# Optimization experiments

Measured on AMD Instinct MI355X. Metric: run time of the kernel, lower is better.

## Reference

```python
import jax, jax.numpy as jnp
import numpy as np

B, N, DEG, F_IN, D = 32, 1024, 16, 8, 64

def setup_inputs() -> dict:
    key = jax.random.key(0)
    ks = jax.random.split(key, 24)
    T = B * N
    E = B * N * DEG
    x = jax.random.normal(ks[0], (T, F_IN), dtype=jnp.float32)
    # edges confined within each graph (block-diagonal batched graph)
    off = (jnp.arange(B) * N)[:, None]
    src = jax.random.randint(ks[1], (B, N * DEG), 0, N) + off
    dst = jax.random.randint(ks[2], (B, N * DEG), 0, N) + off
    edge_index = jnp.stack([src.reshape(-1), dst.reshape(-1)]).astype(jnp.int64)
    reachable = jax.random.randint(ks[3], (T,), 0, 2, dtype=jnp.int32)
    s = 0.1
    p = lambda k, shp: jax.random.normal(k, shp, dtype=jnp.float32) * s
    return {
        'x': x, 'edge_index': edge_index, 'reachable': reachable,
        'Wl0': p(ks[4], (D, F_IN)), 'Wr0': p(ks[5], (D, F_IN)),
        'att0': p(ks[6], (D,)), 'b0': p(ks[7], (D,)),
        'Wl': p(ks[8], (4, D, D)), 'Wr': p(ks[9], (4, D, D)),
        'att': p(ks[10], (4, D)), 'b': p(ks[11], (4, D)),
        't6w': p(ks[12], (D, D)), 't6b': p(ks[13], (D,)),
        't7w': p(ks[14], (D, D)), 't7b': p(ks[15], (D,)),
        't5pw': p(ks[16], (1, 2 * D)), 't5pb': p(ks[17], (1,)),
        't5vw': p(ks[18], (1, 2 * D)), 't5vb': p(ks[19], (1,)),
        'pw': p(ks[20], (1, 1)), 'pb': p(ks[21], (1,)),
        'vw': p(ks[22], (1, 1)), 'vb': p(ks[23], (1,)),
        'n_per_graph': N,
    }

def reference(x, edge_index, reachable, Wl0, Wr0, att0, b0, Wl, Wr, att, b,
              t6w, t6b, t7w, t7b, t5pw, t5pb, t5vw, t5vb, pw, pb, vw, vb,
              n_per_graph):
    T = x.shape[0]
    n = int(n_per_graph)
    bsz = T // n
    d = Wl0.shape[0]
    # GATv2Conv adds self loops by default
    loop = jnp.arange(T)
    src = jnp.concatenate([edge_index[0], loop])
    dst = jnp.concatenate([edge_index[1], loop])

    def gatv2(h, WlK, WrK, a, bb):
        xl = h @ WlK.T                                  # [T, d]
        xr = h @ WrK.T
        e = jax.nn.leaky_relu(xl[src] + xr[dst], 0.2) @ a  # [E]
        emax = jax.ops.segment_max(e, dst, num_segments=T)
        ee = jnp.exp(e - emax[dst])
        denom = jax.ops.segment_sum(ee, dst, num_segments=T)
        alpha = ee / denom[dst]                         # edge softmax per target
        return jax.ops.segment_sum(alpha[:, None] * xl[src], dst, num_segments=T) + bb

    h = gatv2(x, Wl0, Wr0, att0, b0)
    for k in range(Wl.shape[0]):  # ReLU between layers, none after last
        h = gatv2(jax.nn.relu(h), Wl[k], Wr[k], att[k], b[k])
    mu_raw = h                                          # [T, d]

    # scatter_mean pooling per graph + repeat_interleave back to nodes
    mu_mp = mu_raw.reshape(bsz, n, d).mean(axis=1)      # [B, d]
    mu_mp_exp = jnp.repeat(mu_mp, n, axis=0)            # [T, d]

    g = mu_mp_exp @ t6w.T + t6b
    l = mu_raw @ t7w.T + t7b
    rep = jax.nn.relu(jnp.concatenate([g, l], axis=1))  # [T, 2d]

    prob_logits = rep @ t5pw.T + t5pb                   # [T, 1]
    logits = (prob_logits * pw[0, 0] + pb[0]).reshape(bsz, n, 1)

    q = (rep @ t5vw.T + t5vb)[:, 0]                     # [T]
    q = jnp.where(reachable.astype(bool), q, jnp.float32(-1e20))
    v = q.reshape(bsz, n).max(axis=1, keepdims=True)    # [B, 1]
    value = v * vw[0, 0] + vb[0]
    return logits, value
```

## Files before the change

### kernel.cpp

```cpp
#include <hip/hip_runtime.h>
#include <hip/hip_bf16.h>

typedef unsigned short u16;

#define T_NODES 32768
#define NPG 1024
#define BGR 32
#define D 64
#define FIN 8
#define SLOTS 64

typedef __attribute__((ext_vector_type(8))) short short8v;
typedef __attribute__((ext_vector_type(4))) float floatx4;
typedef __attribute__((ext_vector_type(2))) float f32x2;

__device__ __forceinline__ float bf2f(u16 u){ return __uint_as_float(((unsigned)u) << 16); }
__device__ __forceinline__ u16 f2bf(float f){
    __hip_bfloat16 h = __float2bfloat16(f);
    return *reinterpret_cast<u16*>(&h);
}
__device__ __forceinline__ f32x2 lo_hi(unsigned w){
    f32x2 r;
    r[0] = __uint_as_float(w << 16);
    r[1] = __uint_as_float(w & 0xffff0000u);
    return r;
}
__device__ __forceinline__ f32x2 lrelu2(f32x2 v){
    return __builtin_elementwise_max(v, v * 0.2f);
}
__device__ __forceinline__ short8v pack_bf8(float4 a, float4 b){
    short8v r;
    r[0]=(short)f2bf(a.x); r[1]=(short)f2bf(a.y);
    r[2]=(short)f2bf(a.z); r[3]=(short)f2bf(a.w);
    r[4]=(short)f2bf(b.x); r[5]=(short)f2bf(b.y);
    r[6]=(short)f2bf(b.z); r[7]=(short)f2bf(b.w);
    return r;
}

__device__ __forceinline__ unsigned fenc(float f){
    unsigned b = __float_as_uint(f);
    return (b & 0x80000000u) ? ~b : (b | 0x80000000u);
}
__device__ __forceinline__ float fdec(unsigned k){
    unsigned b = (k & 0x80000000u) ? (k ^ 0x80000000u) : ~k;
    return __uint_as_float(b);
}

template<int CTRL, int RM, int BM>
__device__ __forceinline__ float dpp_add(float x){
    int y = __builtin_amdgcn_update_dpp(0, __float_as_int(x), CTRL, RM, BM, false);
    return x + __int_as_float(y);
}
__device__ __forceinline__ float wave_sum63(float x){
    x = dpp_add<0x111,0xf,0xf>(x);
    x = dpp_add<0x112,0xf,0xf>(x);
    x = dpp_add<0x114,0xf,0xe>(x);
    x = dpp_add<0x118,0xf,0xc>(x);
    x = dpp_add<0x142,0xa,0xf>(x);
    x = dpp_add<0x143,0xc,0xf>(x);
    return x;
}
__device__ __forceinline__ float wave_sum_bcast(float x){
    return __int_as_float(__builtin_amdgcn_readlane(__float_as_int(wave_sum63(x)), 63));
}
__device__ __forceinline__ float row_ror_add(float x){
    x = dpp_add<0x121,0xf,0xf>(x);
    x = dpp_add<0x122,0xf,0xf>(x);
    x = dpp_add<0x124,0xf,0xf>(x);
    x = dpp_add<0x128,0xf,0xf>(x);
    return x;
}

__device__ __forceinline__ void edge_body(uint2 uv, bool valid,
        f32x2 a01, f32x2 a23, f32x2 xr01, f32x2 xr23,
        f32x2& acc01, f32x2& acc23, float& l){
    f32x2 x01 = lo_hi(uv.x);
    f32x2 x23 = lo_hi(uv.y);
    f32x2 v01 = lrelu2(x01 + xr01);
    f32x2 v23 = lrelu2(x23 + xr23);
    f32x2 e2 = v01 * a01 + v23 * a23;
    float e = e2[0] + e2[1];
    e = row_ror_add(e);
    float q = valid ? __expf(e) : 0.f;
    acc01 += q * x01;
    acc23 += q * x23;
    l += q;
}

__device__ __forceinline__ void node_edge(const u16* __restrict__ xlin,
        const int* __restrict__ colSh, int eb, int t, int deg, int sub4,
        f32x2 a01, f32x2 a23, f32x2 xr01, f32x2 xr23,
        f32x2& acc01, f32x2& acc23, float& l){
    int nEdge = deg + 1;
    for (int j0 = 0; j0 < nEdge; j0 += 8){
        uint2 u[8];
        #pragma unroll
        for (int i = 0; i < 8; i++){
            int j = j0 + i;
            int jc = (j < nEdge) ? j : (nEdge-1);
            int s = (jc < deg) ? colSh[eb + jc] : t;
            u[i] = *(const uint2*)&xlin[((size_t)(unsigned)s << 6) + sub4];
        }
        #pragma unroll
        for (int i = 0; i < 8; i++)
            edge_body(u[i], j0 + i < nEdge, a01, a23, xr01, xr23, acc01, acc23, l);
    }
}

__global__ void countscat_kernel(const int* __restrict__ src, const int* __restrict__ dst,
                                 int* __restrict__ counts, int* __restrict__ col64, int E){
    int i = blockIdx.x*blockDim.x + threadIdx.x;
    if (i < E){
        int d = dst[i];
        int slot = atomicAdd(&counts[d], 1);
        if (slot < SLOTS) col64[((size_t)d << 6) + slot] = src[i];
    }
}

__global__ void lin0_kernel(const float* __restrict__ x, const float* __restrict__ Wl0,
                            const float* __restrict__ Wr0,
                            u16* __restrict__ xlb, u16* __restrict__ xrb,
                            int* __restrict__ counts, float* __restrict__ muAcc,
                            unsigned* __restrict__ vslot, int* __restrict__ done){
    __shared__ float wl[D][FIN+1];
    __shared__ float wr[D][FIN+1];
    __shared__ float xs[32][FIN];
    int tid = threadIdx.x;
    int blk = blockIdx.x;
    int gidx = blk*256 + tid;
    if (gidx < T_NODES) counts[gidx] = 0;
    if (gidx < BGR*D)   muAcc[gidx] = 0.f;
    if (gidx < BGR){ vslot[gidx] = 0u; done[gidx] = 0; }
    int rowBase = (blk & 7)*4096 + (blk >> 3)*32;
    for (int i = tid; i < D*FIN; i += 256){
        wl[i>>3][i&7] = Wl0[i];
        wr[i>>3][i&7] = Wr0[i];
    }
    xs[tid>>3][tid&7] = x[rowBase*FIN + tid];
    __syncthreads();
    int wave = tid >> 6, lane = tid & 63;
    int rb = rowBase + wave*8;
    #pragma unroll
    for (int r = 0; r < 8; r++){
        float al = 0.f, ar = 0.f;
        int lr = wave*8 + r;
        #pragma unroll
        for (int k = 0; k < FIN; k++){
            float xv = xs[lr][k];
            al = fmaf(xv, wl[lane][k], al);
            ar = fmaf(xv, wr[lane][k], ar);
        }
        xlb[(size_t)(rb+r)*D + lane] = f2bf(al);
        xrb[(size_t)(rb+r)*D + lane] = f2bf(ar);
    }
}

__global__ __launch_bounds__(256) void el_kernel(
        const u16* __restrict__ xlin, const u16* __restrict__ xrin,
        const float* __restrict__ att, const float* __restrict__ bias,
        const int* __restrict__ counts, const int* __restrict__ col64,
        const float* __restrict__ Wl, const float* __restrict__ Wr,
        u16* __restrict__ xlout, u16* __restrict__ xrout){
    __shared__ __align__(16) u16 hs[16][80];
    __shared__ __align__(16) int colSh[16*SLOTS];
    __shared__ int cnt[16];
    int tid = threadIdx.x, blk = blockIdx.x;
    int rowBase = (blk & 7)*4096 + (blk >> 3)*16;
    if (tid < 16){
        int c = counts[rowBase + tid];
        cnt[tid] = c < SLOTS ? c : SLOTS;
    }
    *(int4*)&colSh[tid*4] = *(const int4*)&col64[((size_t)rowBase << 6) + tid*4];
    __syncthreads();
    int wave = tid >> 6, lane = tid & 63;
    int g = lane >> 4, sub4 = (lane & 15) << 2;
    int ln = wave*4 + g;
    int t  = rowBase + ln;
    f32x2 a01 = { att[sub4],   att[sub4+1] };
    f32x2 a23 = { att[sub4+2], att[sub4+3] };
    float4 b4 = *(const float4*)&bias[sub4];
    uint2 xru = *(const uint2*)&xrin[((size_t)t << 6) + sub4];
    f32x2 xr01 = lo_hi(xru.x), xr23 = lo_hi(xru.y);
    int deg = cnt[ln];
    f32x2 acc01 = {0.f,0.f}, acc23 = {0.f,0.f};
    float l = 0.f;
    node_edge(xlin, colSh, ln*SLOTS, t, deg, sub4,
              a01, a23, xr01, xr23, acc01, acc23, l);
    float rl = __frcp_rn(l);
    ushort4 hb;
    hb.x = f2bf(fmaxf(fmaf(acc01[0], rl, b4.x), 0.f));
    hb.y = f2bf(fmaxf(fmaf(acc01[1], rl, b4.y), 0.f));
    hb.z = f2bf(fmaxf(fmaf(acc23[0], rl, b4.z), 0.f));
    hb.w = f2bf(fmaxf(fmaf(acc23[1], rl, b4.w), 0.f));
    *(ushort4*)&hs[ln][sub4] = hb;
    int lw = lane & 15, lg = lane >> 4, kb = lg*8;
    int colw = (wave << 4) + lw;
    const float* wl0 = &Wl[colw*D + kb];
    const float* wr0 = &Wr[colw*D + kb];
    short8v bl0 = pack_bf8(*(const float4*)wl0,        *(const float4*)(wl0+4));
    short8v bl1 = pack_bf8(*(const float4*)(wl0+32),   *(const float4*)(wl0+36));
    short8v br0 = pack_bf8(*(const float4*)wr0,        *(const float4*)(wr0+4));
    short8v br1 = pack_bf8(*(const float4*)(wr0+32),   *(const float4*)(wr0+36));
    __syncthreads();
    short8v a0 = *(const short8v*)&hs[lw][kb];
    short8v a1 = *(const short8v*)&hs[lw][32 + kb];
    floatx4 cl = {0.f,0.f,0.f,0.f}, cr = {0.f,0.f,0.f,0.f};
    cl = __builtin_amdgcn_mfma_f32_16x16x32_bf16(a0, bl0, cl, 0, 0, 0);
    cl = __builtin_amdgcn_mfma_f32_16x16x32_bf16(a1, bl1, cl, 0, 0, 0);
    cr = __builtin_amdgcn_mfma_f32_16x16x32_bf16(a0, br0, cr, 0, 0, 0);
    cr = __builtin_amdgcn_mfma_f32_16x16x32_bf16(a1, br1, cr, 0, 0, 0);
    size_t rb = (size_t)(rowBase + lg*4);
    #pragma unroll
    for (int j = 0; j < 4; j++){
        xlout[(rb + j)*D + colw] = f2bf(cl[j]);
        xrout[(rb + j)*D + colw] = f2bf(cr[j]);
    }
}

__global__ __launch_bounds__(256) void e4_kernel(
        const u16* __restrict__ xlin, const u16* __restrict__ xrin,
        const float* __restrict__ att, const float* __restrict__ bias,
        const int* __restrict__ counts, const int* __restrict__ col64,
        float* __restrict__ hout, float* __restrict__ muAcc){
    __shared__ __align__(16) int colSh[16*SLOTS];
    __shared__ int cnt[16];
    __shared__ float red[16][D];
    int tid = threadIdx.x, blk = blockIdx.x;
    int rowBase = (blk & 7)*4096 + (blk >> 3)*16;
    if (tid < 16){
        int c = counts[rowBase + tid];
        cnt[tid] = c < SLOTS ? c : SLOTS;
    }
    *(int4*)&colSh[tid*4] = *(const int4*)&col64[((size_t)rowBase << 6) + tid*4];
    __syncthreads();
    int wave = tid >> 6, lane = tid & 63;
    int g = lane >> 4, sub4 = (lane & 15) << 2;
    int ln = wave*4 + g;
    int t  = rowBase + ln;
    f32x2 a01 = { att[sub4],   att[sub4+1] };
    f32x2 a23 = { att[sub4+2], att[sub4+3] };
    float4 b4 = *(const float4*)&bias[sub4];
    uint2 xru = *(const uint2*)&xrin[((size_t)t << 6) + sub4];
    f32x2 xr01 = lo_hi(xru.x), xr23 = lo_hi(xru.y);
    int deg = cnt[ln];
    f32x2 acc01 = {0.f,0.f}, acc23 = {0.f,0.f};
    float l = 0.f;
    node_edge(xlin, colSh, ln*SLOTS, t, deg, sub4,
              a01, a23, xr01, xr23, acc01, acc23, l);
    float rl = __frcp_rn(l);
    float4 hv;
    hv.x = fmaf(acc01[0], rl, b4.x);
    hv.y = fmaf(acc01[1], rl, b4.y);
    hv.z = fmaf(acc23[0], rl, b4.z);
    hv.w = fmaf(acc23[1], rl, b4.w);
    *(float4*)&hout[(size_t)t*D + sub4] = hv;
    *(float4*)&red[ln][sub4] = hv;
    __syncthreads();
    if (wave == 0){
        float s = 0.f;
        #pragma unroll
        for (int n = 0; n < 16; n++) s += red[n][lane];
        atomicAdd(&muAcc[(rowBase >> 10)*D + lane], s);
    }
}

__global__ __launch_bounds__(256) void final_kernel(const float* __restrict__ h,
                             const float* __restrict__ muAcc,
                             const float* __restrict__ t6w, const float* __restrict__ t6b,
                             const float* __restrict__ t7w, const float* __restrict__ t7b,
                             const float* __restrict__ t5pw, const float* __restrict__ t5pb,
                             const float* __restrict__ t5vw, const float* __restrict__ t5vb,
                             const float* __restrict__ pw, const float* __restrict__ pb,
                             const float* __restrict__ vw, const float* __restrict__ vb,
                             const int* __restrict__ reachable,
                             unsigned* __restrict__ vslot, int* __restrict__ done,
                             float* __restrict__ out_logits, float* __restrict__ out_value){
    __shared__ __align__(16) float hs[D][68];
    __shared__ __align__(16) float ws[D][68];
    __shared__ float ppar[D][17];
    __shared__ float qpar[D][17];
    __shared__ float PgQg[2];
    int tid = threadIdx.x;
    int blk = blockIdx.x;
    int rowBase = (blk & 7)*4096 + (blk >> 3)*64;
    int b = rowBase >> 10;
    for (int i = tid; i < D*D; i += 256) ws[i>>6][i&63] = t6w[i];
    if (tid < D) hs[0][tid] = muAcc[b*D + tid] * (1.f/NPG);
    __syncthreads();
    if (tid < D){
        int d = tid;
        float g = t6b[d];
        #pragma unroll
        for (int k = 0; k < D; k++) g = fmaf(hs[0][k], ws[d][k], g);
        g = fmaxf(g, 0.f);
        float pp = wave_sum_bcast(g * t5pw[d]);
        float qq = wave_sum_bcast(g * t5vw[d]);
        if (d == 0){ PgQg[0] = pp; PgQg[1] = qq; }
    }
    __syncthreads();
    for (int i = tid; i < D*D; i += 256){
        int r = i >> 6, c = i & 63;
        hs[r][c] = h[(size_t)rowBase*D + i];
        ws[r][c] = t7w[i];
    }
    __syncthreads();
    int ty = tid >> 4, tx = tid & 15;
    int r0 = ty * 4;
    float acc[4][4];
    #pragma unroll
    for (int i = 0; i < 4; i++)
        #pragma unroll
        for (int j = 0; j < 4; j++) acc[i][j] = 0.f;
    for (int k = 0; k < D; k += 4){
        float4 hv[4], wv[4];
        #pragma unroll
        for (int i = 0; i < 4; i++){
            hv[i] = *(const float4*)&hs[r0+i][k];
            wv[i] = *(const float4*)&ws[tx + 16*i][k];
        }
        #pragma unroll
        for (int i = 0; i < 4; i++)
            #pragma unroll
            for (int j = 0; j < 4; j++)
                acc[i][j] += hv[i].x*wv[j].x + hv[i].y*wv[j].y
                           + hv[i].z*wv[j].z + hv[i].w*wv[j].w;
    }
    float bc[4], pwc[4], qwc[4];
    #pragma unroll
    for (int j = 0; j < 4; j++){
        int c = tx + 16*j;
        bc[j]  = t7b[c];
        pwc[j] = t5pw[D + c];
        qwc[j] = t5vw[D + c];
    }
    #pragma unroll
    for (int i = 0; i < 4; i++){
        float sp = 0.f, sq = 0.f;
        #pragma unroll
        for (int j = 0; j < 4; j++){
            float lv = fmaxf(acc[i][j] + bc[j], 0.f);
            sp = fmaf(lv, pwc[j], sp);
            sq = fmaf(lv, qwc[j], sq);
        }
        ppar[r0+i][tx] = sp;
        qpar[r0+i][tx] = sq;
    }
    __syncthreads();
    if (tid < 64){
        int t = rowBase + tid;
        float sp = 0.f, sq = 0.f;
        #pragma unroll
        for (int c = 0; c < 16; c++){ sp += ppar[tid][c]; sq += qpar[tid][c]; }
        float prob = PgQg[0] + sp + t5pb[0];
        out_logits[t] = prob * pw[0] + pb[0];
        float q = PgQg[1] + sq + t5vb[0];
        if (!reachable[t]) q = -1e20f;
        float m = q;
        #pragma unroll
        for (int o = 1; o < 64; o <<= 1) m = fmaxf(m, __shfl_xor(m, o, 64));
        if (tid == 0){
            atomicMax(&vslot[b], fenc(m));
            __threadfence();
            int ticket = atomicAdd(&done[b], 1);
            if (ticket == (NPG/64) - 1){
                unsigned k = atomicOr(&vslot[b], 0u);
                out_value[b] = fdec(k)*vw[0] + vb[0];
            }
        }
    }
}

extern "C" void kernel_launch(void* const* d_in, const int* in_sizes, int n_in,
                              void* d_out, int out_size, void* d_ws, size_t ws_size,
                              hipStream_t stream){
    const float* x          = (const float*)d_in[0];
    const int*   edge_index = (const int*)d_in[1];
    const int*   reachable  = (const int*)d_in[2];
    const float* Wl0 = (const float*)d_in[3];
    const float* Wr0 = (const float*)d_in[4];
    const float* att0= (const float*)d_in[5];
    const float* b0  = (const float*)d_in[6];
    const float* Wl  = (const float*)d_in[7];
    const float* Wr  = (const float*)d_in[8];
    const float* att = (const float*)d_in[9];
    const float* bb  = (const float*)d_in[10];
    const float* t6w = (const float*)d_in[11];
    const float* t6b = (const float*)d_in[12];
    const float* t7w = (const float*)d_in[13];
    const float* t7b = (const float*)d_in[14];
    const float* t5pw= (const float*)d_in[15];
    const float* t5pb= (const float*)d_in[16];
    const float* t5vw= (const float*)d_in[17];
    const float* t5vb= (const float*)d_in[18];
    const float* pw  = (const float*)d_in[19];
    const float* pb  = (const float*)d_in[20];
    const float* vw  = (const float*)d_in[21];
    const float* vb  = (const float*)d_in[22];

    int E = in_sizes[1] / 2;
    const int* esrc = edge_index;
    const int* edst = edge_index + E;

    char* ws = (char*)d_ws;
    float* h    = (float*)(ws);
    u16* xlbA   = (u16*)(ws + (size_t)T_NODES*D*4);
    u16* xrbA   = (u16*)((char*)xlbA + (size_t)T_NODES*D*2);
    u16* xlbB   = (u16*)((char*)xrbA + (size_t)T_NODES*D*2);
    u16* xrbB   = (u16*)((char*)xlbB + (size_t)T_NODES*D*2);
    int* counts = (int*)((char*)xrbB + (size_t)T_NODES*D*2);
    int* col64  = (int*)((char*)counts + (size_t)(T_NODES+16)*4);
    float* muAcc= (float*)((char*)col64 + (size_t)T_NODES*SLOTS*4);
    unsigned* vslot = (unsigned*)((char*)muAcc + (size_t)BGR*D*4);
    int* done   = (int*)((char*)vslot + (size_t)BGR*4);

    lin0_kernel<<<T_NODES/32, 256, 0, stream>>>(x, Wl0, Wr0, xlbA, xrbA,
                                                counts, muAcc, vslot, done);
    countscat_kernel<<<(E+255)/256, 256, 0, stream>>>(esrc, edst, counts, col64, E);

    el_kernel<<<T_NODES/16, 256, 0, stream>>>(xlbA, xrbA, att0, b0, counts, col64,
                                              Wl + 0*D*D, Wr + 0*D*D, xlbB, xrbB);
    el_kernel<<<T_NODES/16, 256, 0, stream>>>(xlbB, xrbB, att + 0*D, bb + 0*D, counts, col64,
                                              Wl + 1*D*D, Wr + 1*D*D, xlbA, xrbA);
    el_kernel<<<T_NODES/16, 256, 0, stream>>>(xlbA, xrbA, att + 1*D, bb + 1*D, counts, col64,
                                              Wl + 2*D*D, Wr + 2*D*D, xlbB, xrbB);
    el_kernel<<<T_NODES/16, 256, 0, stream>>>(xlbB, xrbB, att + 2*D, bb + 2*D, counts, col64,
                                              Wl + 3*D*D, Wr + 3*D*D, xlbA, xrbA);
    e4_kernel<<<T_NODES/16, 256, 0, stream>>>(xlbA, xrbA, att + 3*D, bb + 3*D, counts, col64,
                                              h, muAcc);

    final_kernel<<<T_NODES/64, 256, 0, stream>>>(h, muAcc, t6w, t6b, t7w, t7b,
                                                 t5pw, t5pb, t5vw, t5vb, pw, pb, vw, vb,
                                                 reachable, vslot, done,
                                                 (float*)d_out, (float*)d_out + T_NODES);
}
```

Measured before the change: 242.9 us.

## Fuse last GAT layer with readout head using inter-block per-graph flag sync

Merges the final GATv2 layer kernel with the readout kernel so each block of 64 nodes keeps its layer output in shared memory, instead of writing h to global memory and reading it back. The per-graph mean-pool result is computed by the last-arriving block of each graph, which publishes the global projection through a flag that the other blocks spin on. This removes one launch and the h round trip. In exchange it relies on all blocks of a graph being co-resident to avoid deadlock, and it cuts block count and raises shared memory per block.

```diff
diff --git a/kernel.cpp b/kernel.cpp
--- a/kernel.cpp
+++ b/kernel.cpp
@@ -88,7 +88,7 @@
 }
 
 __device__ __forceinline__ void node_edge(const u16* __restrict__ xlin,
-        const int* __restrict__ colSh, int eb, int t, int deg, int sub4,
+        const int* colSh, int eb, int t, int deg, int sub4,
         f32x2 a01, f32x2 a23, f32x2 xr01, f32x2 xr23,
         f32x2& acc01, f32x2& acc23, float& l){
     int nEdge = deg + 1;
@@ -121,7 +121,8 @@
                             const float* __restrict__ Wr0,
                             u16* __restrict__ xlb, u16* __restrict__ xrb,
                             int* __restrict__ counts, float* __restrict__ muAcc,
-                            unsigned* __restrict__ vslot, int* __restrict__ done){
+                            unsigned* __restrict__ vslot, int* __restrict__ done,
+                            int* __restrict__ pgdone, int* __restrict__ pgflag){
     __shared__ float wl[D][FIN+1];
     __shared__ float wr[D][FIN+1];
     __shared__ float xs[32][FIN];
@@ -130,7 +131,7 @@
     int gidx = blk*256 + tid;
     if (gidx < T_NODES) counts[gidx] = 0;
     if (gidx < BGR*D)   muAcc[gidx] = 0.f;
-    if (gidx < BGR){ vslot[gidx] = 0u; done[gidx] = 0; }
+    if (gidx < BGR){ vslot[gidx] = 0u; done[gidx] = 0; pgdone[gidx] = 0; pgflag[gidx] = 0; }
     int rowBase = (blk & 7)*4096 + (blk >> 3)*32;
     for (int i = tid; i < D*FIN; i += 256){
         wl[i>>3][i&7] = Wl0[i];
@@ -217,93 +218,101 @@
     }
 }
 
-__global__ __launch_bounds__(256) void e4_kernel(
+__global__ __launch_bounds__(256) void e4final_kernel(
         const u16* __restrict__ xlin, const u16* __restrict__ xrin,
         const float* __restrict__ att, const float* __restrict__ bias,
         const int* __restrict__ counts, const int* __restrict__ col64,
-        float* __restrict__ hout, float* __restrict__ muAcc){
-    __shared__ __align__(16) int colSh[16*SLOTS];
-    __shared__ int cnt[16];
-    __shared__ float red[16][D];
+        const float* __restrict__ t6w, const float* __restrict__ t6b,
+        const float* __restrict__ t7w, const float* __restrict__ t7b,
+        const float* __restrict__ t5pw, const float* __restrict__ t5pb,
+        const float* __restrict__ t5vw, const float* __restrict__ t5vb,
+        const float* __restrict__ pw, const float* __restrict__ pb,
+        const float* __restrict__ vw, const float* __restrict__ vb,
+        const int* __restrict__ reachable,
+        float* __restrict__ muAcc, unsigned* __restrict__ vslot,
+        int* __restrict__ done, int* __restrict__ pgdone,
+        int* __restrict__ pgflag, float* __restrict__ gPQ,
+        float* __restrict__ out_logits, float* __restrict__ out_value){
+    __shared__ __align__(16) char arena[43776];
+    __shared__ float muS[D];
+    __shared__ float PgQgS[2];
+    __shared__ int isLastS;
+    float* hfin  = (float*)arena;
+    int*   colSh = (int*)  (arena + 17408);
+    int*   cnt   = (int*)  (arena + 33792);
+    float* wsH   = (float*)(arena + 17408);
+    float* ppar  = (float*)(arena + 34816);
+    float* qpar  = (float*)(arena + 39168);
+
     int tid = threadIdx.x, blk = blockIdx.x;
-    int rowBase = (blk & 7)*4096 + (blk >> 3)*16;
-    if (tid < 16){
+    int rowBase = (blk & 7)*4096 + (blk >> 3)*64;
+    int b = rowBase >> 10;
+    if (tid < 64){
         int c = counts[rowBase + tid];
         cnt[tid] = c < SLOTS ? c : SLOTS;
     }
-    *(int4*)&colSh[tid*4] = *(const int4*)&col64[((size_t)rowBase << 6) + tid*4];
+    for (int i = tid; i < 1024; i += 256)
+        *(int4*)&colSh[i*4] = *(const int4*)&col64[((size_t)rowBase << 6) + i*4];
     __syncthreads();
     int wave = tid >> 6, lane = tid & 63;
     int g = lane >> 4, sub4 = (lane & 15) << 2;
-    int ln = wave*4 + g;
-    int t  = rowBase + ln;
+    int gid = wave*4 + g;
     f32x2 a01 = { att[sub4],   att[sub4+1] };
     f32x2 a23 = { att[sub4+2], att[sub4+3] };
     float4 b4 = *(const float4*)&bias[sub4];
-    uint2 xru = *(const uint2*)&xrin[((size_t)t << 6) + sub4];
-    f32x2 xr01 = lo_hi(xru.x), xr23 = lo_hi(xru.y);
-    int deg = cnt[ln];
-    f32x2 acc01 = {0.f,0.f}, acc23 = {0.f,0.f};
-    float l = 0.f;
-    node_edge(xlin, colSh, ln*SLOTS, t, deg, sub4,
-              a01, a23, xr01, xr23, acc01, acc23, l);
-    float rl = __frcp_rn(l);
-    float4 hv;
-    hv.x = fmaf(acc01[0], rl, b4.x);
-    hv.y = fmaf(acc01[1], rl, b4.y);
-    hv.z = fmaf(acc23[0], rl, b4.z);
-    hv.w = fmaf(acc23[1], rl, b4.w);
-    *(float4*)&hout[(size_t)t*D + sub4] = hv;
-    *(float4*)&red[ln][sub4] = hv;
-    __syncthreads();
+    for (int n = 0; n < 4; n++){
+        int ln = gid + n*16;
+        int t  = rowBase + ln;
+        uint2 xru = *(const uint2*)&xrin[((size_t)t << 6) + sub4];
+        f32x2 xr01 = lo_hi(xru.x), xr23 = lo_hi(xru.y);
+        int deg = cnt[ln];
+        f32x2 acc01 = {0.f,0.f}, acc23 = {0.f,0.f};
+        float l = 0.f;
+        node_edge(xlin, colSh, ln*SLOTS, t, deg, sub4,
+                  a01, a23, xr01, xr23, acc01, acc23, l);
+        float rl = __frcp_rn(l);
+        float4 hv;
+        hv.x = fmaf(acc01[0], rl, b4.x);
+        hv.y = fmaf(acc01[1], rl, b4.y);
+        hv.z = fmaf(acc23[0], rl, b4.z);
+        hv.w = fmaf(acc23[1], rl, b4.w);
+        *(float4*)&hfin[ln*68 + sub4] = hv;
+    }
+    __syncthreads();
+    for (int i = tid; i < D*D; i += 256) wsH[(i>>6)*68 + (i&63)] = t7w[i];
     if (wave == 0){
         float s = 0.f;
         #pragma unroll
-        for (int n = 0; n < 16; n++) s += red[n][lane];
-        atomicAdd(&muAcc[(rowBase >> 10)*D + lane], s);
-    }
-}
-
-__global__ __launch_bounds__(256) void final_kernel(const float* __restrict__ h,
-                             const float* __restrict__ muAcc,
-                             const float* __restrict__ t6w, const float* __restrict__ t6b,
-                             const float* __restrict__ t7w, const float* __restrict__ t7b,
-                             const float* __restrict__ t5pw, const float* __restrict__ t5pb,
-                             const float* __restrict__ t5vw, const float* __restrict__ t5vb,
-                             const float* __restrict__ pw, const float* __restrict__ pb,
-                             const float* __restrict__ vw, const float* __restrict__ vb,
-                             const int* __restrict__ reachable,
-                             unsigned* __restrict__ vslot, int* __restrict__ done,
-                             float* __restrict__ out_logits, float* __restrict__ out_value){
-    __shared__ __align__(16) float hs[D][68];
-    __shared__ __align__(16) float ws[D][68];
-    __shared__ float ppar[D][17];
-    __shared__ float qpar[D][17];
-    __shared__ float PgQg[2];
-    int tid = threadIdx.x;
-    int blk = blockIdx.x;
-    int rowBase = (blk & 7)*4096 + (blk >> 3)*64;
-    int b = rowBase >> 10;
-    for (int i = tid; i < D*D; i += 256) ws[i>>6][i&63] = t6w[i];
-    if (tid < D) hs[0][tid] = muAcc[b*D + tid] * (1.f/NPG);
-    __syncthreads();
-    if (tid < D){
-        int d = tid;
-        float g = t6b[d];
-        #pragma unroll
-        for (int k = 0; k < D; k++) g = fmaf(hs[0][k], ws[d][k], g);
-        g = fmaxf(g, 0.f);
-        float pp = wave_sum_bcast(g * t5pw[d]);
-        float qq = wave_sum_bcast(g * t5vw[d]);
-        if (d == 0){ PgQg[0] = pp; PgQg[1] = qq; }
-    }
-    __syncthreads();
-    for (int i = tid; i < D*D; i += 256){
-        int r = i >> 6, c = i & 63;
-        hs[r][c] = h[(size_t)rowBase*D + i];
-        ws[r][c] = t7w[i];
-    }
-    __syncthreads();
+        for (int nn = 0; nn < 64; nn++) s += hfin[nn*68 + lane];
+        atomicAdd(&muAcc[b*D + lane], s);
+    }
+    __syncthreads();
+    if (tid == 0){
+        int tk = atomicAdd(&pgdone[b], 1);
+        isLastS = (tk == (NPG/64) - 1);
+    }
+    __syncthreads();
+    if (isLastS){
+        if (tid < D)
+            muS[tid] = __hip_atomic_load(&muAcc[b*D + tid], __ATOMIC_RELAXED,
+                                         __HIP_MEMORY_SCOPE_AGENT) * (1.f/NPG);
+        __syncthreads();
+        if (tid < D){
+            int d = tid;
+            float gg = t6b[d];
+            #pragma unroll
+            for (int k = 0; k < D; k++) gg = fmaf(muS[k], t6w[d*D + k], gg);
+            gg = fmaxf(gg, 0.f);
+            float pp = wave_sum_bcast(gg * t5pw[d]);
+            float qq = wave_sum_bcast(gg * t5vw[d]);
+            if (d == 0){
+                __hip_atomic_store(&gPQ[b*2],   pp, __ATOMIC_RELAXED, __HIP_MEMORY_SCOPE_AGENT);
+                __hip_atomic_store(&gPQ[b*2+1], qq, __ATOMIC_RELAXED, __HIP_MEMORY_SCOPE_AGENT);
+                asm volatile("s_waitcnt vmcnt(0)" ::: "memory");
+                __hip_atomic_store(&pgflag[b], 1, __ATOMIC_RELAXED, __HIP_MEMORY_SCOPE_AGENT);
+            }
+        }
+    }
     int ty = tid >> 4, tx = tid & 15;
     int r0 = ty * 4;
     float acc[4][4];
@@ -315,8 +324,8 @@
         float4 hv[4], wv[4];
         #pragma unroll
         for (int i = 0; i < 4; i++){
-            hv[i] = *(const float4*)&hs[r0+i][k];
-            wv[i] = *(const float4*)&ws[tx + 16*i][k];
+            hv[i] = *(const float4*)&hfin[(r0+i)*68 + k];
+            wv[i] = *(const float4*)&wsH[(tx + 16*i)*68 + k];
         }
         #pragma unroll
         for (int i = 0; i < 4; i++)
@@ -342,28 +351,37 @@
             sp = fmaf(lv, pwc[j], sp);
             sq = fmaf(lv, qwc[j], sq);
         }
-        ppar[r0+i][tx] = sp;
-        qpar[r0+i][tx] = sq;
+        ppar[(r0+i)*17 + tx] = sp;
+        qpar[(r0+i)*17 + tx] = sq;
+    }
+    __syncthreads();
+    if (tid == 0){
+        while (__hip_atomic_load(&pgflag[b], __ATOMIC_RELAXED,
+                                 __HIP_MEMORY_SCOPE_AGENT) == 0)
+            __builtin_amdgcn_s_sleep(16);
+        PgQgS[0] = __hip_atomic_load(&gPQ[b*2],   __ATOMIC_RELAXED, __HIP_MEMORY_SCOPE_AGENT);
+        PgQgS[1] = __hip_atomic_load(&gPQ[b*2+1], __ATOMIC_RELAXED, __HIP_MEMORY_SCOPE_AGENT);
     }
     __syncthreads();
     if (tid < 64){
         int t = rowBase + tid;
         float sp = 0.f, sq = 0.f;
         #pragma unroll
-        for (int c = 0; c < 16; c++){ sp += ppar[tid][c]; sq += qpar[tid][c]; }
-        float prob = PgQg[0] + sp + t5pb[0];
+        for (int c = 0; c < 16; c++){ sp += ppar[tid*17 + c]; sq += qpar[tid*17 + c]; }
+        float prob = PgQgS[0] + sp + t5pb[0];
         out_logits[t] = prob * pw[0] + pb[0];
-        float q = PgQg[1] + sq + t5vb[0];
+        float q = PgQgS[1] + sq + t5vb[0];
         if (!reachable[t]) q = -1e20f;
         float m = q;
         #pragma unroll
         for (int o = 1; o < 64; o <<= 1) m = fmaxf(m, __shfl_xor(m, o, 64));
         if (tid == 0){
             atomicMax(&vslot[b], fenc(m));
-            __threadfence();
+            asm volatile("s_waitcnt vmcnt(0)" ::: "memory");
             int ticket = atomicAdd(&done[b], 1);
             if (ticket == (NPG/64) - 1){
-                unsigned k = atomicOr(&vslot[b], 0u);
+                unsigned k = __hip_atomic_load(&vslot[b], __ATOMIC_RELAXED,
+                                               __HIP_MEMORY_SCOPE_AGENT);
                 out_value[b] = fdec(k)*vw[0] + vb[0];
             }
         }
@@ -402,19 +420,22 @@
     const int* edst = edge_index + E;
 
     char* ws = (char*)d_ws;
-    float* h    = (float*)(ws);
-    u16* xlbA   = (u16*)(ws + (size_t)T_NODES*D*4);
-    u16* xrbA   = (u16*)((char*)xlbA + (size_t)T_NODES*D*2);
-    u16* xlbB   = (u16*)((char*)xrbA + (size_t)T_NODES*D*2);
-    u16* xrbB   = (u16*)((char*)xlbB + (size_t)T_NODES*D*2);
-    int* counts = (int*)((char*)xrbB + (size_t)T_NODES*D*2);
-    int* col64  = (int*)((char*)counts + (size_t)(T_NODES+16)*4);
-    float* muAcc= (float*)((char*)col64 + (size_t)T_NODES*SLOTS*4);
-    unsigned* vslot = (unsigned*)((char*)muAcc + (size_t)BGR*D*4);
-    int* done   = (int*)((char*)vslot + (size_t)BGR*4);
+    u16* xlbA   = (u16*)ws;
+    u16* xrbA   = xlbA + (size_t)T_NODES*D;
+    u16* xlbB   = xrbA + (size_t)T_NODES*D;
+    u16* xrbB   = xlbB + (size_t)T_NODES*D;
+    int* counts = (int*)(xrbB + (size_t)T_NODES*D);
+    int* col64  = counts + T_NODES + 16;
+    float* muAcc= (float*)(col64 + (size_t)T_NODES*SLOTS);
+    unsigned* vslot = (unsigned*)(muAcc + BGR*D);
+    int* done   = (int*)(vslot + BGR);
+    int* pgdone = done + BGR;
+    int* pgflag = pgdone + BGR;
+    float* gPQ  = (float*)(pgflag + BGR);
 
     lin0_kernel<<<T_NODES/32, 256, 0, stream>>>(x, Wl0, Wr0, xlbA, xrbA,
-                                                counts, muAcc, vslot, done);
+                                                counts, muAcc, vslot, done,
+                                                pgdone, pgflag);
     countscat_kernel<<<(E+255)/256, 256, 0, stream>>>(esrc, edst, counts, col64, E);
 
     el_kernel<<<T_NODES/16, 256, 0, stream>>>(xlbA, xrbA, att0, b0, counts, col64,
@@ -425,11 +446,11 @@
                                               Wl + 2*D*D, Wr + 2*D*D, xlbB, xrbB);
     el_kernel<<<T_NODES/16, 256, 0, stream>>>(xlbB, xrbB, att + 2*D, bb + 2*D, counts, col64,
                                               Wl + 3*D*D, Wr + 3*D*D, xlbA, xrbA);
-    e4_kernel<<<T_NODES/16, 256, 0, stream>>>(xlbA, xrbA, att + 3*D, bb + 3*D, counts, col64,
-                                              h, muAcc);
-
-    final_kernel<<<T_NODES/64, 256, 0, stream>>>(h, muAcc, t6w, t6b, t7w, t7b,
-                                                 t5pw, t5pb, t5vw, t5vb, pw, pb, vw, vb,
-                                                 reachable, vslot, done,
-                                                 (float*)d_out, (float*)d_out + T_NODES);
-}
+
+    e4final_kernel<<<T_NODES/64, 256, 0, stream>>>(xlbA, xrbA, att + 3*D, bb + 3*D,
+                                                   counts, col64, t6w, t6b, t7w, t7b,
+                                                   t5pw, t5pb, t5vw, t5vb, pw, pb, vw, vb,
+                                                   reachable, muAcc, vslot, done,
+                                                   pgdone, pgflag, gPQ,
+                                                   (float*)d_out, (float*)d_out + T_NODES);
+}
```

Result: faster. 233.6 us (-3.8%).
